# Kernel optimization log

Measured on AMD Instinct MI355X. Metric: run time of the kernel, lower is better.

The kernel has to match this reference:

```python
import jax, jax.numpy as jnp
import numpy as np

SEQ_LEN = 8192
IN = 180      # input_size * window_size = 6 * 30
HID = 64
OUT = 10      # forecast_steps
HPM_H = 2
HPM_IN = OUT + 2 * HID + IN  # 318


def setup_inputs() -> dict:
    key = jax.random.key(0)
    ks = jax.random.split(key, 16)
    u = lambda k, shape, s: jax.random.uniform(k, shape, jnp.float32, -s, s)
    s0 = 1.0 / np.sqrt(HID)
    return {
        "input": jax.random.normal(ks[0], (SEQ_LEN, 1, IN), jnp.float32),
        "W_ih0": u(ks[1], (4 * HID, IN), s0),
        "W_hh0": u(ks[2], (4 * HID, HID), s0),
        "b_ih0": u(ks[3], (4 * HID,), s0),
        "b_hh0": u(ks[4], (4 * HID,), s0),
        "W_ih1": u(ks[5], (4 * HID, HID), s0),
        "W_hh1": u(ks[6], (4 * HID, HID), s0),
        "b_ih1": u(ks[7], (4 * HID,), s0),
        "b_hh1": u(ks[8], (4 * HID,), s0),
        "W_lin": u(ks[9], (OUT, HID), s0),
        "b_lin": u(ks[10], (OUT,), s0),
        "W_h1": u(ks[11], (HPM_H, HPM_IN), 1.0 / np.sqrt(HPM_IN)),
        "b_h1": u(ks[12], (HPM_H,), 1.0 / np.sqrt(HPM_IN)),
        "W_h2": u(ks[13], (IN, HPM_H), 1.0 / np.sqrt(HPM_H)),
        "b_h2": u(ks[14], (IN,), 1.0 / np.sqrt(HPM_H)),
    }


def _lstm_cell(x, h, c, Wih, Whh, bih, bhh):
    g = x @ Wih.T + bih + h @ Whh.T + bhh
    i, f, gg, o = jnp.split(g, 4, axis=-1)
    c2 = jax.nn.sigmoid(f) * c + jax.nn.sigmoid(i) * jnp.tanh(gg)
    h2 = jax.nn.sigmoid(o) * jnp.tanh(c2)
    return h2, c2


def _minmax(x):
    mn = jnp.min(x, axis=0)
    mx = jnp.max(x, axis=0)
    return (x - mn) / (mx - mn + 1e-6)


def reference(input, W_ih0, W_hh0, b_ih0, b_hh0, W_ih1, W_hh1, b_ih1, b_hh1,
              W_lin, b_lin, W_h1, b_h1, W_h2, b_h2):
    S, B, _ = input.shape  # B must be 1 (module structurally requires it)
    z = jnp.zeros((B, HID), input.dtype)

    def step(carry, x):
        h0, c0, h1, c1 = carry
        old_h = h0  # h_t0 before update (old_hts)
        h0, c0 = _lstm_cell(x, h0, c0, W_ih0, W_hh0, b_ih0, b_hh0)
        h1, c1 = _lstm_cell(h0, h1, c1, W_ih1, W_hh1, b_ih1, b_hh1)
        out = h1 @ W_lin.T + b_lin
        return (h0, c0, h1, c1), (out, old_h)

    _, (outs, old_hts) = jax.lax.scan(step, (z, z, z, z), input)
    outputs = outs[:, 0, :]                      # (S, OUT)
    old_hts_n = _minmax(old_hts[:, 0, :])        # (S, HID)
    # mc_dropout=False path: output_hiddens and out_xs are all zeros
    hiddens = jnp.zeros((S, HID), input.dtype)   # min-max of zeros is zeros
    output_data = jnp.concatenate(
        [outputs, hiddens, input[:, 0, :], old_hts_n], axis=1)  # (S, 318)

    def neg_hpm(X):  # F = out_xs - G = -G since out_xs == 0
        return -(jnp.tanh(X @ W_h1.T + b_h1) @ W_h2.T + b_h2)

    F, vjp = jax.vjp(neg_hpm, output_data)       # (S, IN)
    AllF_x = vjp(jnp.ones_like(F))[0]            # grad of sum(F) wrt output_data, (S, 318)
    return outputs, F, AllF_x
```

## Files before the change

### kernel.cpp

```cpp
#include <hip/hip_runtime.h>
#include <hip/hip_bf16.h>
#include <float.h>

#define SEQ   8192
#define INW   180
#define HID   64
#define G4    256
#define OUTW  10
#define XW    318

typedef float f32x4 __attribute__((ext_vector_type(4)));
typedef _Float16 h16x2 __attribute__((ext_vector_type(2)));
typedef unsigned int uint32;

__device__ __forceinline__ float frcp(float x)   { return __builtin_amdgcn_rcpf(x); }
__device__ __forceinline__ float tanhf_f(float x){ return 1.0f - 2.0f * frcp(1.0f + __expf(2.0f * x)); }
__device__ __forceinline__ float gate_act(float x, bool isg) {
    float xx = isg ? 2.0f * x : x;
    float s  = frcp(1.0f + __expf(-xx));
    return isg ? 2.0f * s - 1.0f : s;
}

template<int CTRL>
__device__ __forceinline__ float dpp_bcast(float x) {
    return __int_as_float(__builtin_amdgcn_update_dpp(
        0, __float_as_int(x), CTRL, 0xF, 0xF, true));
}

__device__ __forceinline__ float fdot2h(h16x2 a, h16x2 b, float c) {
#if __has_builtin(__builtin_amdgcn_fdot2)
    return __builtin_amdgcn_fdot2(a, b, c, false);
#else
    asm("v_dot2_f32_f16 %0, %1, %2, %3" : "=v"(c) : "v"(a), "v"(b), "0"(c));
    return c;
#endif
}

__device__ __forceinline__ h16x2 h2f(float f)   { return __builtin_bit_cast(h16x2, f); }
__device__ __forceinline__ h16x2 h2u(uint32 u)  { return __builtin_bit_cast(h16x2, u); }
__device__ __forceinline__ uint32 pack_h2(float lo, float hi) {
    h16x2 h; h.x = (_Float16)lo; h.y = (_Float16)hi;
    return __builtin_bit_cast(uint32, h);
}

__device__ __forceinline__ f32x4 opaque_load4(const float* p) {
    f32x4 v;
    asm volatile("global_load_dwordx4 %0, %1, off" : "=v"(v) : "v"(p));
    return v;
}

__global__ __launch_bounds__(256) void k_packw(
    const float* __restrict__ Whh0, const float* __restrict__ Wih1,
    const float* __restrict__ Whh1,
    uint32* __restrict__ w0h, uint32* __restrict__ w1ah, uint32* __restrict__ w1bh)
{
    const int gid = blockIdx.x * 256 + threadIdx.x;
    const int mat = gid >> 13;
    const int i   = gid & 8191;
    const int r   = i >> 5, k2 = i & 31;
    const float* S = (mat == 0) ? Whh0 : (mat == 1) ? Wih1 : Whh1;
    uint32*      D = (mat == 0) ? w0h  : (mat == 1) ? w1ah : w1bh;
    D[i] = pack_h2(S[r * 64 + 2 * k2], S[r * 64 + 2 * k2 + 1]);
}

#define PRE_TS 16
__global__ __launch_bounds__(256) void k_precompute(
    const float* __restrict__ x, const float* __restrict__ Wih0,
    const float* __restrict__ bih0, const float* __restrict__ bhh0,
    float* __restrict__ pre)
{
    __shared__ float xT[INW][PRE_TS];
    const int t  = threadIdx.x;
    const int rr = (t & 3) * 64 + (t >> 2);
    const int s0 = blockIdx.x * PRE_TS;
    for (int i = t; i < PRE_TS * INW; i += 256) {
        int s = i / INW, k = i % INW;
        xT[k][s] = x[s0 * INW + i];
    }
    __syncthreads();
    float acc[PRE_TS];
    const float b = bih0[rr] + bhh0[rr];
#pragma unroll
    for (int s = 0; s < PRE_TS; ++s) acc[s] = b;
    for (int k = 0; k < INW; ++k) {
        float w = Wih0[rr * INW + k];
#pragma unroll
        for (int s = 0; s < PRE_TS; ++s) acc[s] += w * xT[k][s];
    }
#pragma unroll
    for (int s = 0; s < PRE_TS; ++s) pre[(s0 + s) * G4 + t] = acc[s];
}

#define DOT4(A0, A1, A2, A3, WQ, HQ)                         \
    A0 = fdot2h(h2f((WQ).x), h2u((HQ).x), A0);               \
    A1 = fdot2h(h2f((WQ).y), h2u((HQ).y), A1);               \
    A2 = fdot2h(h2f((WQ).z), h2u((HQ).z), A2);               \
    A3 = fdot2h(h2f((WQ).w), h2u((HQ).w), A3);

__global__ __launch_bounds__(512) __attribute__((amdgpu_num_vgpr(168)))
void k_lstm_seq(
    const float* __restrict__ pre,
    const uint32* __restrict__ w0h,
    const uint32* __restrict__ w1ah,
    const uint32* __restrict__ w1bh,
    const float* __restrict__ bih1, const float* __restrict__ bhh1,
    float* __restrict__ oldh, float* __restrict__ h1h)
{
    const int t = threadIdx.x;

    __shared__ __attribute__((aligned(16))) uint32 h0p[2][32];
    __shared__ __attribute__((aligned(16))) uint32 h1p[2][32];
    if (t < 32) { h0p[0][t] = 0u; h0p[1][t] = 0u; h1p[0][t] = 0u; h1p[1][t] = 0u; }
    if (t < 64) oldh[t] = 0.0f;
    __syncthreads();

    if (t < 256) {
        const int q = t, g = q & 3, u = q >> 2, r = g * 64 + u;
        const bool isg = (g == 2);

        f32x4 w[8];
        {
            const float* W = (const float*)(w0h + r * 32);
#pragma unroll
            for (int j = 0; j < 8; ++j) w[j] = opaque_load4(W + 4 * j);
            asm volatile("s_waitcnt vmcnt(0)" ::: "memory");
        }
        float c0 = 0.f;
        float preval = pre[q];
        for (int s = 0; s <= SEQ; ++s) {
            if (s < SEQ) {
                const int p = s & 1, pn = p ^ 1;
                const int sn = (s + 1 < SEQ) ? (s + 1) : s;
                float prenext = pre[sn * G4 + q];

                const uint4* Hp = (const uint4*)&h0p[p][0];
                float a0 = preval, a1 = 0.f, a2 = 0.f, a3 = 0.f;
                {
                    uint4 hq0 = Hp[0], hq1 = Hp[1], hq2 = Hp[2], hq3 = Hp[3];
                    DOT4(a0, a1, a2, a3, w[0], hq0)
                    DOT4(a0, a1, a2, a3, w[1], hq1)
                    DOT4(a0, a1, a2, a3, w[2], hq2)
                    DOT4(a0, a1, a2, a3, w[3], hq3)
                }
                __builtin_amdgcn_sched_barrier(0);
                {
                    uint4 hq4 = Hp[4], hq5 = Hp[5], hq6 = Hp[6], hq7 = Hp[7];
                    DOT4(a0, a1, a2, a3, w[4], hq4)
                    DOT4(a0, a1, a2, a3, w[5], hq5)
                    DOT4(a0, a1, a2, a3, w[6], hq6)
                    DOT4(a0, a1, a2, a3, w[7], hq7)
                }
                float a  = gate_act((a0 + a1) + (a2 + a3), isg);
                float ai = dpp_bcast<0x00>(a);
                float af = dpp_bcast<0x55>(a);
                float ag = dpp_bcast<0xAA>(a);
                float ao = dpp_bcast<0xFF>(a);
                c0 = fmaf(af, c0, ai * ag);
                float h0n = ao * tanhf_f(c0);
                float hpart = __shfl_xor(h0n, 4);
                if ((q & 7) == 0) h0p[pn][u >> 1] = pack_h2(h0n, hpart);
                if ((q & 3) == 1 && s + 1 < SEQ) oldh[(s + 1) * HID + u] = h0n;
                preval = prenext;
            }
            asm volatile("s_waitcnt lgkmcnt(0)" ::: "memory");
            __builtin_amdgcn_s_barrier();
            asm volatile("" ::: "memory");
        }
    } else {
        const int q = t - 256, g = q & 3, u = q >> 2, r = g * 64 + u;
        const bool isg = (g == 2);

        f32x4 wa[8], wb[8];
        {
            const float* Wa = (const float*)(w1ah + r * 32);
            const float* Wb = (const float*)(w1bh + r * 32);
#pragma unroll
            for (int j = 0; j < 8; ++j) wa[j] = opaque_load4(Wa + 4 * j);
#pragma unroll
            for (int j = 0; j < 8; ++j) wb[j] = opaque_load4(Wb + 4 * j);
            asm volatile("s_waitcnt vmcnt(0)" ::: "memory");
        }
        const float b1 = bih1[r] + bhh1[r];
        float c1 = 0.f;
        for (int s = 0; s <= SEQ; ++s) {
            if (s >= 1) {
                const int p = s & 1, pn = p ^ 1;
                const uint4* H0 = (const uint4*)&h0p[p][0];
                const uint4* H1 = (const uint4*)&h1p[p][0];
                float a0 = b1, a1 = 0.f, a2 = 0.f, a3 = 0.f;
                {
                    uint4 hq0 = H0[0], hq1 = H0[1], hq2 = H0[2], hq3 = H0[3];
                    DOT4(a0, a1, a2, a3, wa[0], hq0)
                    DOT4(a0, a1, a2, a3, wa[1], hq1)
                    DOT4(a0, a1, a2, a3, wa[2], hq2)
                    DOT4(a0, a1, a2, a3, wa[3], hq3)
                }
                __builtin_amdgcn_sched_barrier(0);
                {
                    uint4 hq4 = H0[4], hq5 = H0[5], hq6 = H0[6], hq7 = H0[7];
                    DOT4(a0, a1, a2, a3, wa[4], hq4)
                    DOT4(a0, a1, a2, a3, wa[5], hq5)
                    DOT4(a0, a1, a2, a3, wa[6], hq6)
                    DOT4(a0, a1, a2, a3, wa[7], hq7)
                }
                __builtin_amdgcn_sched_barrier(0);
                {
                    uint4 hq0 = H1[0], hq1 = H1[1], hq2 = H1[2], hq3 = H1[3];
                    DOT4(a0, a1, a2, a3, wb[0], hq0)
                    DOT4(a0, a1, a2, a3, wb[1], hq1)
                    DOT4(a0, a1, a2, a3, wb[2], hq2)
                    DOT4(a0, a1, a2, a3, wb[3], hq3)
                }
                __builtin_amdgcn_sched_barrier(0);
                {
                    uint4 hq4 = H1[4], hq5 = H1[5], hq6 = H1[6], hq7 = H1[7];
                    DOT4(a0, a1, a2, a3, wb[4], hq4)
                    DOT4(a0, a1, a2, a3, wb[5], hq5)
                    DOT4(a0, a1, a2, a3, wb[6], hq6)
                    DOT4(a0, a1, a2, a3, wb[7], hq7)
                }
                float a  = gate_act((a0 + a1) + (a2 + a3), isg);
                float ai = dpp_bcast<0x00>(a);
                float af = dpp_bcast<0x55>(a);
                float ag = dpp_bcast<0xAA>(a);
                float ao = dpp_bcast<0xFF>(a);
                c1 = fmaf(af, c1, ai * ag);
                float h1n = ao * tanhf_f(c1);
                float hpart = __shfl_xor(h1n, 4);
                if ((q & 7) == 0) h1p[pn][u >> 1] = pack_h2(h1n, hpart);
                if ((q & 3) == 1) h1h[(s - 1) * HID + u] = h1n;
            }
            asm volatile("s_waitcnt lgkmcnt(0)" ::: "memory");
            __builtin_amdgcn_s_barrier();
            asm volatile("" ::: "memory");
        }
    }
}

__global__ __launch_bounds__(256) void k_minmax1(
    const float* __restrict__ oldh, float* __restrict__ pmn, float* __restrict__ pmx)
{
    const int t = threadIdx.x, b = blockIdx.x;
    float vmn = FLT_MAX, vmx = -FLT_MAX;
    for (int i = t; i < 128 * HID; i += 256) {
        float v = oldh[b * 128 * HID + i];
        vmn = fminf(vmn, v); vmx = fmaxf(vmx, v);
    }
    __shared__ float smn[256], smx[256];
    smn[t] = vmn; smx[t] = vmx;
    __syncthreads();
    if (t < 64) {
        float m0 = fminf(fminf(smn[t], smn[t + 64]), fminf(smn[t + 128], smn[t + 192]));
        float m1 = fmaxf(fmaxf(smx[t], smx[t + 64]), fmaxf(smx[t + 128], smx[t + 192]));
        pmn[b * 64 + t] = m0; pmx[b * 64 + t] = m1;
    }
}

__global__ __launch_bounds__(256) void k_minmax2(
    const float* __restrict__ pmn, const float* __restrict__ pmx,
    float* __restrict__ mn, float* __restrict__ mx)
{
    const int t = threadIdx.x, col = t & 63, chunk = t >> 6;
    float vmn = FLT_MAX, vmx = -FLT_MAX;
    for (int r = chunk * 16; r < chunk * 16 + 16; ++r) {
        vmn = fminf(vmn, pmn[r * 64 + col]);
        vmx = fmaxf(vmx, pmx[r * 64 + col]);
    }
    __shared__ float smn[256], smx[256];
    smn[t] = vmn; smx[t] = vmx;
    __syncthreads();
    if (t < 64) {
        mn[t] = fminf(fminf(smn[t], smn[t + 64]), fminf(smn[t + 128], smn[t + 192]));
        mx[t] = fmaxf(fmaxf(smx[t], smx[t + 64]), fmaxf(smx[t + 128], smx[t + 192]));
    }
}

__global__ __launch_bounds__(256) void k_finalize(
    const float* __restrict__ h1h, const float* __restrict__ oldh,
    const float* __restrict__ x,
    const float* __restrict__ Wlin, const float* __restrict__ blin,
    const float* __restrict__ Wh1,  const float* __restrict__ bh1,
    const float* __restrict__ Wh2,  const float* __restrict__ bh2,
    const float* __restrict__ mn,   const float* __restrict__ mx,
    float* __restrict__ dout)
{
    float* out_o = dout;
    float* out_F = dout + SEQ * OUTW;
    float* out_A = dout + SEQ * (OUTW + INW);

    const int wave = threadIdx.x >> 6, lane = threadIdx.x & 63;
    const int row  = blockIdx.x * 4 + wave;

    __shared__ float Xs[4][XW + 2];
    __shared__ float h1sh[4][HID];

    h1sh[wave][lane] = h1h[row * HID + lane];
    float mnv = mn[lane], mxv = mx[lane];
    Xs[wave][254 + lane] = (oldh[row * HID + lane] - mnv) * frcp(mxv - mnv + 1e-6f);
    Xs[wave][10 + lane]  = 0.0f;
    for (int c = lane; c < INW; c += 64) Xs[wave][74 + c] = x[row * INW + c];
    __syncthreads();

    if (lane < OUTW) {
        float o = blin[lane];
#pragma unroll
        for (int k = 0; k < HID; ++k) o += Wlin[lane * HID + k] * h1sh[wave][k];
        Xs[wave][lane] = o;
        out_o[row * OUTW + lane] = o;
    }
    __syncthreads();

    float z0 = 0.f, z1 = 0.f, s0 = 0.f, s1 = 0.f;
    for (int c = lane; c < XW; c += 64) {
        float xv = Xs[wave][c];
        z0 += xv * Wh1[c];
        z1 += xv * Wh1[XW + c];
    }
    for (int j = lane; j < INW; j += 64) {
        s0 += Wh2[j * 2 + 0];
        s1 += Wh2[j * 2 + 1];
    }
#pragma unroll
    for (int off = 32; off; off >>= 1) {
        z0 += __shfl_xor(z0, off); z1 += __shfl_xor(z1, off);
        s0 += __shfl_xor(s0, off); s1 += __shfl_xor(s1, off);
    }
    const float t0 = tanhf_f(z0 + bh1[0]);
    const float t1 = tanhf_f(z1 + bh1[1]);
    const float a0 = -s0 * (1.0f - t0 * t0);
    const float a1 = -s1 * (1.0f - t1 * t1);

    for (int c = lane; c < INW; c += 64)
        out_F[row * INW + c] = -(t0 * Wh2[c * 2 + 0] + t1 * Wh2[c * 2 + 1] + bh2[c]);
    for (int c = lane; c < XW; c += 64)
        out_A[row * XW + c] = a0 * Wh1[c] + a1 * Wh1[XW + c];
}

extern "C" void kernel_launch(void* const* d_in, const int* in_sizes, int n_in,
                              void* d_out, int out_size, void* d_ws, size_t ws_size,
                              hipStream_t stream)
{
    const float* input = (const float*)d_in[0];
    const float* Wih0  = (const float*)d_in[1];
    const float* Whh0  = (const float*)d_in[2];
    const float* bih0  = (const float*)d_in[3];
    const float* bhh0  = (const float*)d_in[4];
    const float* Wih1  = (const float*)d_in[5];
    const float* Whh1  = (const float*)d_in[6];
    const float* bih1  = (const float*)d_in[7];
    const float* bhh1  = (const float*)d_in[8];
    const float* Wlin  = (const float*)d_in[9];
    const float* blin  = (const float*)d_in[10];
    const float* Wh1   = (const float*)d_in[11];
    const float* bh1   = (const float*)d_in[12];
    const float* Wh2   = (const float*)d_in[13];
    const float* bh2   = (const float*)d_in[14];

    float* ws   = (float*)d_ws;
    float* pre  = ws;
    float* oldh = pre  + SEQ * G4;
    float* h1h  = oldh + SEQ * HID;
    float* pmn  = h1h  + SEQ * HID;
    float* pmx  = pmn  + 64 * 64;
    float* mn   = pmx  + 64 * 64;
    float* mx   = mn   + 64;
    uint32* w0h  = (uint32*)(mx + 64);
    uint32* w1ah = w0h  + G4 * 32;
    uint32* w1bh = w1ah + G4 * 32;
    float* out  = (float*)d_out;

    hipLaunchKernelGGL(k_packw, dim3(96), dim3(256), 0, stream,
                       Whh0, Wih1, Whh1, w0h, w1ah, w1bh);
    hipLaunchKernelGGL(k_precompute, dim3(SEQ / PRE_TS), dim3(256), 0, stream,
                       input, Wih0, bih0, bhh0, pre);
    hipLaunchKernelGGL(k_lstm_seq, dim3(1), dim3(512), 0, stream,
                       pre, w0h, w1ah, w1bh, bih1, bhh1, oldh, h1h);
    hipLaunchKernelGGL(k_minmax1, dim3(64), dim3(256), 0, stream, oldh, pmn, pmx);
    hipLaunchKernelGGL(k_minmax2, dim3(1), dim3(256), 0, stream, pmn, pmx, mn, mx);
    hipLaunchKernelGGL(k_finalize, dim3(SEQ / 4), dim3(256), 0, stream,
                       h1h, oldh, input, Wlin, blin, Wh1, bh1, Wh2, bh2, mn, mx, out);
}
```

Baseline: 4.313 ms.

## Run both LSTM layers sequentially in one 256-thread block instead of split warps

The recurrent kernel previously used 512 threads: one half ran layer 0 and the other ran layer 1 one step behind, with a single barrier per step. Now 256 threads hold all three weight sets in registers and compute layer 0, hit a barrier, then compute layer 1, with a second barrier. The aim is fewer waves per barrier, less SIMD sharing and a fresher layer-0 state for layer 1. The cost is losing the overlap between the two layers, so each step's critical path becomes both layers plus two barriers.

Result: slower. 6.963 ms (+61.4%).

```diff
diff --git a/kernel.cpp b/kernel.cpp
--- a/kernel.cpp
+++ b/kernel.cpp
@@ -97,7 +97,7 @@
     A2 = fdot2h(h2f((WQ).z), h2u((HQ).z), A2);               \
     A3 = fdot2h(h2f((WQ).w), h2u((HQ).w), A3);
 
-__global__ __launch_bounds__(512) __attribute__((amdgpu_num_vgpr(168)))
+__global__ __launch_bounds__(256, 1)
 void k_lstm_seq(
     const float* __restrict__ pre,
     const uint32* __restrict__ w0h,
@@ -107,133 +107,121 @@
     float* __restrict__ oldh, float* __restrict__ h1h)
 {
     const int t = threadIdx.x;
+    const int q = t, g = q & 3, u = q >> 2, r = g * 64 + u;
+    const bool isg = (g == 2);
 
     __shared__ __attribute__((aligned(16))) uint32 h0p[2][32];
     __shared__ __attribute__((aligned(16))) uint32 h1p[2][32];
     if (t < 32) { h0p[0][t] = 0u; h0p[1][t] = 0u; h1p[0][t] = 0u; h1p[1][t] = 0u; }
     if (t < 64) oldh[t] = 0.0f;
-    __syncthreads();
-
-    if (t < 256) {
-        const int q = t, g = q & 3, u = q >> 2, r = g * 64 + u;
-        const bool isg = (g == 2);
-
-        f32x4 w[8];
+
+    f32x4 w0[8], wa[8], wb[8];
+    {
+        const float* W0 = (const float*)(w0h  + r * 32);
+        const float* Wa = (const float*)(w1ah + r * 32);
+        const float* Wb = (const float*)(w1bh + r * 32);
+#pragma unroll
+        for (int j = 0; j < 8; ++j) w0[j] = opaque_load4(W0 + 4 * j);
+#pragma unroll
+        for (int j = 0; j < 8; ++j) wa[j] = opaque_load4(Wa + 4 * j);
+#pragma unroll
+        for (int j = 0; j < 8; ++j) wb[j] = opaque_load4(Wb + 4 * j);
+        asm volatile("s_waitcnt vmcnt(0)" ::: "memory");
+    }
+    const float b1 = bih1[r] + bhh1[r];
+    float c0 = 0.f, c1 = 0.f;
+    float preval = pre[q];
+    __syncthreads();
+
+    for (int s = 0; s < SEQ; ++s) {
+        const int p = s & 1, pn = p ^ 1;
+
         {
-            const float* W = (const float*)(w0h + r * 32);
-#pragma unroll
-            for (int j = 0; j < 8; ++j) w[j] = opaque_load4(W + 4 * j);
-            asm volatile("s_waitcnt vmcnt(0)" ::: "memory");
+            const int sn = (s + 1 < SEQ) ? (s + 1) : s;
+            float prenext = pre[sn * G4 + q];
+
+            const uint4* Hp = (const uint4*)&h0p[p][0];
+            float a0 = preval, a1 = 0.f, a2 = 0.f, a3 = 0.f;
+            {
+                uint4 hq0 = Hp[0], hq1 = Hp[1], hq2 = Hp[2], hq3 = Hp[3];
+                DOT4(a0, a1, a2, a3, w0[0], hq0)
+                DOT4(a0, a1, a2, a3, w0[1], hq1)
+                DOT4(a0, a1, a2, a3, w0[2], hq2)
+                DOT4(a0, a1, a2, a3, w0[3], hq3)
+            }
+            __builtin_amdgcn_sched_barrier(0);
+            {
+                uint4 hq4 = Hp[4], hq5 = Hp[5], hq6 = Hp[6], hq7 = Hp[7];
+                DOT4(a0, a1, a2, a3, w0[4], hq4)
+                DOT4(a0, a1, a2, a3, w0[5], hq5)
+                DOT4(a0, a1, a2, a3, w0[6], hq6)
+                DOT4(a0, a1, a2, a3, w0[7], hq7)
+            }
+            float a  = gate_act((a0 + a1) + (a2 + a3), isg);
+            float ai = dpp_bcast<0x00>(a);
+            float af = dpp_bcast<0x55>(a);
+            float ag = dpp_bcast<0xAA>(a);
+            float ao = dpp_bcast<0xFF>(a);
+            c0 = fmaf(af, c0, ai * ag);
+            float h0n = ao * tanhf_f(c0);
+            float hpart = __shfl_xor(h0n, 4);
+            if ((q & 7) == 0) h0p[pn][u >> 1] = pack_h2(h0n, hpart);
+            if ((q & 3) == 1 && s + 1 < SEQ) oldh[(s + 1) * HID + u] = h0n;
+            preval = prenext;
         }
-        float c0 = 0.f;
-        float preval = pre[q];
-        for (int s = 0; s <= SEQ; ++s) {
-            if (s < SEQ) {
-                const int p = s & 1, pn = p ^ 1;
-                const int sn = (s + 1 < SEQ) ? (s + 1) : s;
-                float prenext = pre[sn * G4 + q];
-
-                const uint4* Hp = (const uint4*)&h0p[p][0];
-                float a0 = preval, a1 = 0.f, a2 = 0.f, a3 = 0.f;
-                {
-                    uint4 hq0 = Hp[0], hq1 = Hp[1], hq2 = Hp[2], hq3 = Hp[3];
-                    DOT4(a0, a1, a2, a3, w[0], hq0)
-                    DOT4(a0, a1, a2, a3, w[1], hq1)
-                    DOT4(a0, a1, a2, a3, w[2], hq2)
-                    DOT4(a0, a1, a2, a3, w[3], hq3)
-                }
-                __builtin_amdgcn_sched_barrier(0);
-                {
-                    uint4 hq4 = Hp[4], hq5 = Hp[5], hq6 = Hp[6], hq7 = Hp[7];
-                    DOT4(a0, a1, a2, a3, w[4], hq4)
-                    DOT4(a0, a1, a2, a3, w[5], hq5)
-                    DOT4(a0, a1, a2, a3, w[6], hq6)
-                    DOT4(a0, a1, a2, a3, w[7], hq7)
-                }
-                float a  = gate_act((a0 + a1) + (a2 + a3), isg);
-                float ai = dpp_bcast<0x00>(a);
-                float af = dpp_bcast<0x55>(a);
-                float ag = dpp_bcast<0xAA>(a);
-                float ao = dpp_bcast<0xFF>(a);
-                c0 = fmaf(af, c0, ai * ag);
-                float h0n = ao * tanhf_f(c0);
-                float hpart = __shfl_xor(h0n, 4);
-                if ((q & 7) == 0) h0p[pn][u >> 1] = pack_h2(h0n, hpart);
-                if ((q & 3) == 1 && s + 1 < SEQ) oldh[(s + 1) * HID + u] = h0n;
-                preval = prenext;
-            }
-            asm volatile("s_waitcnt lgkmcnt(0)" ::: "memory");
-            __builtin_amdgcn_s_barrier();
-            asm volatile("" ::: "memory");
+        asm volatile("s_waitcnt lgkmcnt(0)" ::: "memory");
+        __builtin_amdgcn_s_barrier();
+        asm volatile("" ::: "memory");
+
+        {
+            const uint4* H0 = (const uint4*)&h0p[pn][0];
+            const uint4* H1 = (const uint4*)&h1p[p][0];
+            float a0 = b1, a1 = 0.f, a2 = 0.f, a3 = 0.f;
+            {
+                uint4 hq0 = H0[0], hq1 = H0[1], hq2 = H0[2], hq3 = H0[3];
+                DOT4(a0, a1, a2, a3, wa[0], hq0)
+                DOT4(a0, a1, a2, a3, wa[1], hq1)
+                DOT4(a0, a1, a2, a3, wa[2], hq2)
+                DOT4(a0, a1, a2, a3, wa[3], hq3)
+            }
+            __builtin_amdgcn_sched_barrier(0);
+            {
+                uint4 hq4 = H0[4], hq5 = H0[5], hq6 = H0[6], hq7 = H0[7];
+                DOT4(a0, a1, a2, a3, wa[4], hq4)
+                DOT4(a0, a1, a2, a3, wa[5], hq5)
+                DOT4(a0, a1, a2, a3, wa[6], hq6)
+                DOT4(a0, a1, a2, a3, wa[7], hq7)
+            }
+            __builtin_amdgcn_sched_barrier(0);
+            {
+                uint4 hq0 = H1[0], hq1 = H1[1], hq2 = H1[2], hq3 = H1[3];
+                DOT4(a0, a1, a2, a3, wb[0], hq0)
+                DOT4(a0, a1, a2, a3, wb[1], hq1)
+                DOT4(a0, a1, a2, a3, wb[2], hq2)
+                DOT4(a0, a1, a2, a3, wb[3], hq3)
+            }
+            __builtin_amdgcn_sched_barrier(0);
+            {
+                uint4 hq4 = H1[4], hq5 = H1[5], hq6 = H1[6], hq7 = H1[7];
+                DOT4(a0, a1, a2, a3, wb[4], hq4)
+                DOT4(a0, a1, a2, a3, wb[5], hq5)
+                DOT4(a0, a1, a2, a3, wb[6], hq6)
+                DOT4(a0, a1, a2, a3, wb[7], hq7)
+            }
+            float a  = gate_act((a0 + a1) + (a2 + a3), isg);
+            float ai = dpp_bcast<0x00>(a);
+            float af = dpp_bcast<0x55>(a);
+            float ag = dpp_bcast<0xAA>(a);
+            float ao = dpp_bcast<0xFF>(a);
+            c1 = fmaf(af, c1, ai * ag);
+            float h1n = ao * tanhf_f(c1);
+            float hpart = __shfl_xor(h1n, 4);
+            if ((q & 7) == 0) h1p[pn][u >> 1] = pack_h2(h1n, hpart);
+            if ((q & 3) == 1) h1h[s * HID + u] = h1n;
         }
-    } else {
-        const int q = t - 256, g = q & 3, u = q >> 2, r = g * 64 + u;
-        const bool isg = (g == 2);
-
-        f32x4 wa[8], wb[8];
-        {
-            const float* Wa = (const float*)(w1ah + r * 32);
-            const float* Wb = (const float*)(w1bh + r * 32);
-#pragma unroll
-            for (int j = 0; j < 8; ++j) wa[j] = opaque_load4(Wa + 4 * j);
-#pragma unroll
-            for (int j = 0; j < 8; ++j) wb[j] = opaque_load4(Wb + 4 * j);
-            asm volatile("s_waitcnt vmcnt(0)" ::: "memory");
-        }
-        const float b1 = bih1[r] + bhh1[r];
-        float c1 = 0.f;
-        for (int s = 0; s <= SEQ; ++s) {
-            if (s >= 1) {
-                const int p = s & 1, pn = p ^ 1;
-                const uint4* H0 = (const uint4*)&h0p[p][0];
-                const uint4* H1 = (const uint4*)&h1p[p][0];
-                float a0 = b1, a1 = 0.f, a2 = 0.f, a3 = 0.f;
-                {
-                    uint4 hq0 = H0[0], hq1 = H0[1], hq2 = H0[2], hq3 = H0[3];
-                    DOT4(a0, a1, a2, a3, wa[0], hq0)
-                    DOT4(a0, a1, a2, a3, wa[1], hq1)
-                    DOT4(a0, a1, a2, a3, wa[2], hq2)
-                    DOT4(a0, a1, a2, a3, wa[3], hq3)
-                }
-                __builtin_amdgcn_sched_barrier(0);
-                {
-                    uint4 hq4 = H0[4], hq5 = H0[5], hq6 = H0[6], hq7 = H0[7];
-                    DOT4(a0, a1, a2, a3, wa[4], hq4)
-                    DOT4(a0, a1, a2, a3, wa[5], hq5)
-                    DOT4(a0, a1, a2, a3, wa[6], hq6)
-                    DOT4(a0, a1, a2, a3, wa[7], hq7)
-                }
-                __builtin_amdgcn_sched_barrier(0);
-                {
-                    uint4 hq0 = H1[0], hq1 = H1[1], hq2 = H1[2], hq3 = H1[3];
-                    DOT4(a0, a1, a2, a3, wb[0], hq0)
-                    DOT4(a0, a1, a2, a3, wb[1], hq1)
-                    DOT4(a0, a1, a2, a3, wb[2], hq2)
-                    DOT4(a0, a1, a2, a3, wb[3], hq3)
-                }
-                __builtin_amdgcn_sched_barrier(0);
-                {
-                    uint4 hq4 = H1[4], hq5 = H1[5], hq6 = H1[6], hq7 = H1[7];
-                    DOT4(a0, a1, a2, a3, wb[4], hq4)
-                    DOT4(a0, a1, a2, a3, wb[5], hq5)
-                    DOT4(a0, a1, a2, a3, wb[6], hq6)
-                    DOT4(a0, a1, a2, a3, wb[7], hq7)
-                }
-                float a  = gate_act((a0 + a1) + (a2 + a3), isg);
-                float ai = dpp_bcast<0x00>(a);
-                float af = dpp_bcast<0x55>(a);
-                float ag = dpp_bcast<0xAA>(a);
-                float ao = dpp_bcast<0xFF>(a);
-                c1 = fmaf(af, c1, ai * ag);
-                float h1n = ao * tanhf_f(c1);
-                float hpart = __shfl_xor(h1n, 4);
-                if ((q & 7) == 0) h1p[pn][u >> 1] = pack_h2(h1n, hpart);
-                if ((q & 3) == 1) h1h[(s - 1) * HID + u] = h1n;
-            }
-            asm volatile("s_waitcnt lgkmcnt(0)" ::: "memory");
-            __builtin_amdgcn_s_barrier();
-            asm volatile("" ::: "memory");
-        }
+        asm volatile("s_waitcnt lgkmcnt(0)" ::: "memory");
+        __builtin_amdgcn_s_barrier();
+        asm volatile("" ::: "memory");
     }
 }
 
@@ -373,7 +361,7 @@
                        Whh0, Wih1, Whh1, w0h, w1ah, w1bh);
     hipLaunchKernelGGL(k_precompute, dim3(SEQ / PRE_TS), dim3(256), 0, stream,
                        input, Wih0, bih0, bhh0, pre);
-    hipLaunchKernelGGL(k_lstm_seq, dim3(1), dim3(512), 0, stream,
+    hipLaunchKernelGGL(k_lstm_seq, dim3(1), dim3(256), 0, stream,
                        pre, w0h, w1ah, w1bh, bih1, bhh1, oldh, h1h);
     hipLaunchKernelGGL(k_minmax1, dim3(64), dim3(256), 0, stream, oldh, pmn, pmx);
     hipLaunchKernelGGL(k_minmax2, dim3(1), dim3(256), 0, stream, pmn, pmx, mn, mx);
```
